# Kernel optimization log

Hardware: AMD Instinct MI355X
Metric: run time of the kernel (lower is better)

Reference implementation:

```python
import jax, jax.numpy as jnp
import numpy as np

# Module constants derived from default grid_config
D = 59          # depth bins: (60-1)/1
C_OUT = 64
X, Y, Z = 128, 128, 7
STRIDE = 16
GRID_LB = np.array([-51.2, -51.2, -2.5], dtype=np.float32)
GRID_IV = np.array([0.8, 0.8, 1.0], dtype=np.float32)
D0, DSTEP = 1.0, 1.0

B, N, C_IN, H, W = 4, 6, 256, 16, 44


def _voxel_coords():
    xs, ys, zs = np.meshgrid(np.arange(X), np.arange(Y), np.arange(Z), indexing='ij')
    coords = np.stack([xs, ys, zs], axis=-1).reshape(-1, 3).astype(np.float32)
    coords = coords * GRID_IV + GRID_LB  # [V, 3] ego-frame voxel centers
    return coords


def _camera_rig(rng):
    """Realistic 6-camera rig: yawed cameras looking outward, z_cam = forward."""
    c2e = np.zeros((B, N, 4, 4), dtype=np.float32)
    K = np.zeros((B, N, 3, 3), dtype=np.float32)
    for b in range(B):
        for n in range(N):
            a = 2.0 * np.pi * n / N + 0.02 * rng.standard_normal()
            f = np.array([np.cos(a), np.sin(a), 0.0])           # camera forward (z_cam)
            x_cam = np.array([-np.sin(a), np.cos(a), 0.0])      # camera right
            y_cam = np.array([0.0, 0.0, -1.0])                   # camera down
            R = np.stack([x_cam, y_cam, f], axis=1)              # columns = cam axes in ego
            t = 1.0 * f + np.array([0.0, 0.0, 1.5])
            c2e[b, n, :3, :3] = R
            c2e[b, n, :3, 3] = t
            c2e[b, n, 3, 3] = 1.0
            fl = 400.0 + 5.0 * rng.standard_normal()
            K[b, n] = np.array([[fl, 0.0, 352.0], [0.0, fl, 128.0], [0.0, 0.0, 1.0]])
    return c2e, K


def setup_inputs() -> dict:
    key = jax.random.key(0)
    k1, k2, k3 = jax.random.split(key, 3)
    img_feats = jax.random.normal(k1, (B, N, C_IN, H, W), dtype=jnp.float32)
    c2e, K = _camera_rig(np.random.default_rng(0))
    # depth_net: 1x1 conv in_channels -> D + C_OUT
    w_depth = jax.random.normal(k2, (D + C_OUT, C_IN), dtype=jnp.float32) * (1.0 / np.sqrt(C_IN))
    b_depth = jax.random.normal(k3, (D + C_OUT,), dtype=jnp.float32) * 0.01
    return {
        'img_feats': img_feats,
        'cam2ego': jnp.asarray(c2e),
        'cam_intrinsics': jnp.asarray(K),
        'w_depth': w_depth,
        'b_depth': b_depth,
    }


def reference(img_feats, cam2ego, cam_intrinsics, w_depth, b_depth):
    Bc, Nc, C, Hc, Wc = img_feats.shape
    # 1x1 conv == per-pixel linear
    x = jnp.einsum('bnchw,oc->bnhwo', img_feats, w_depth) + b_depth  # [B,N,H,W,D+C_OUT]
    depth = jax.nn.softmax(x[..., :D], axis=-1)                      # [B,N,H,W,D]
    feat = x[..., D:]                                                # [B,N,H,W,C_OUT]

    vox = jnp.asarray(_voxel_coords())                               # [V,3]
    V = vox.shape[0]
    vox_h = jnp.concatenate([vox, jnp.ones((V, 1), vox.dtype)], axis=1)  # [V,4]

    e2c = jnp.linalg.inv(cam2ego)                                    # [B,N,4,4]
    cam = jnp.einsum('bnij,vj->bnvi', e2c, vox_h)[..., :3]           # [B,N,V,3]
    z = cam[..., 2]
    z_safe = jnp.maximum(z, 0.1)
    norm = cam[..., :2] / z_safe[..., None]
    homo = jnp.concatenate([norm, jnp.ones_like(z[..., None])], axis=-1)  # [B,N,V,3]
    img = jnp.einsum('bnij,bnvj->bnvi', cam_intrinsics, homo)[..., :2]
    fc = img / STRIDE                                                # feature-plane coords

    depth_bin = ((z - D0) / DSTEP).astype(jnp.int32)                 # trunc toward 0, matches .long()
    valid = (
        (fc[..., 0] >= 0) & (fc[..., 0] < Wc)
        & (fc[..., 1] >= 0) & (fc[..., 1] < Hc)
        & (z > 0.5)
        & (depth_bin >= 0) & (depth_bin < D)
    )

    u = jnp.clip(fc[..., 0].astype(jnp.int32), 0, Wc - 1)            # [B,N,V]
    v = jnp.clip(fc[..., 1].astype(jnp.int32), 0, Hc - 1)
    d = jnp.clip(depth_bin, 0, D - 1)
    hw = v * Wc + u

    feat_flat = feat.reshape(Bc, Nc, Hc * Wc, C_OUT)
    sampled_feat = jnp.take_along_axis(feat_flat, hw[..., None], axis=2)   # [B,N,V,C_OUT]
    depth_flat = depth.reshape(Bc, Nc, Hc * Wc * D)
    sampled_depth = jnp.take_along_axis(depth_flat, hw * D + d, axis=2)    # [B,N,V]

    wgt = sampled_depth * valid.astype(sampled_depth.dtype)
    # scatter_add at flat_idx == voxel index (identity) -> masked sum over cameras
    bev = jnp.einsum('bnv,bnvc->bvc', wgt, sampled_feat)             # [B,V,C_OUT]
    bev = bev.reshape(Bc, X, Y, Z, C_OUT).sum(axis=3)                # collapse Z
    bev = bev.transpose(0, 3, 2, 1)                                  # [B,C_OUT,Y,X]
    return bev, depth
```

## Files before the change

### kernel.cpp

```cpp
#include <hip/hip_runtime.h>
#include <math.h>

#define D_BINS 59
#define CO     64
#define CI     256
#define NB     4
#define NC     6
#define H_IMG  16
#define W_IMG  44
#define HW     704
#define NPIX   (NB*NC*HW)
#define XD     128
#define YD     128
#define ZD     7
#define NOUT   123

__device__ void inv_rigid(const float* __restrict__ M, float* __restrict__ o) {
    double a = M[0], b = M[1], c = M[2], t0 = M[3];
    double d = M[4], e = M[5], f = M[6], t1 = M[7];
    double g = M[8], h = M[9], ii = M[10], t2 = M[11];
    double A00 = e*ii - f*h, A01 = c*h - b*ii, A02 = b*f - c*e;
    double A10 = f*g - d*ii, A11 = a*ii - c*g, A12 = c*d - a*f;
    double A20 = d*h - e*g,  A21 = b*g - a*h,  A22 = a*e - b*d;
    double det = a*A00 + b*A10 + c*A20;
    double inv = 1.0 / det;
    double r00 = A00*inv, r01 = A01*inv, r02 = A02*inv;
    double r10 = A10*inv, r11 = A11*inv, r12 = A12*inv;
    double r20 = A20*inv, r21 = A21*inv, r22 = A22*inv;
    o[0] = (float)r00; o[1] = (float)r01; o[2]  = (float)r02;
    o[3] = (float)(-(r00*t0 + r01*t1 + r02*t2));
    o[4] = (float)r10; o[5] = (float)r11; o[6]  = (float)r12;
    o[7] = (float)(-(r10*t0 + r11*t1 + r12*t2));
    o[8] = (float)r20; o[9] = (float)r21; o[10] = (float)r22;
    o[11] = (float)(-(r20*t0 + r21*t1 + r22*t2));
}

__global__ __launch_bounds__(256) void k_pre(
    const float* __restrict__ wd, const float* __restrict__ c2e,
    float* __restrict__ wt, float* __restrict__ e2c) {
    const int o = blockIdx.x;
    const int k = threadIdx.x;
    float v = (o < NOUT) ? wd[(size_t)o * CI + k] : 0.f;
    wt[(size_t)k * 128 + o] = v;
    if (blockIdx.x == 0 && k < NB * NC)
        inv_rigid(c2e + k * 16, e2c + k * 12);
}

__global__ __launch_bounds__(512) void k_head(
    const float* __restrict__ img, const float* __restrict__ wt,
    const float* __restrict__ bd, float* __restrict__ depth_out,
    float* __restrict__ feat_ws) {
    __shared__ float smem[8448 + 64];
    float* A_lds = smem;
    float* S = smem + 8448;

    const int px = threadIdx.x;
    const int tid = threadIdx.y * 64 + threadIdx.x;
    const int o0 = __builtin_amdgcn_readfirstlane(threadIdx.y << 4);
    const int p0 = blockIdx.x * 64;
    const int bn = p0 / HW;
    const int hw0 = p0 % HW;
    const float* imgb = img + (size_t)bn * CI * HW + hw0;

    float acc[16];
#pragma unroll
    for (int j = 0; j < 16; ++j) acc[j] = 0.f;

    for (int kc = 0; kc < 4; ++kc) {
#pragma unroll
        for (int it = 0; it < 2; ++it) {
            int idx = tid + it * 512;
            int r = idx >> 4, c4 = idx & 15;
            float4 v = *(const float4*)(imgb + (size_t)(kc * 64 + r) * HW + c4 * 4);
            *(float4*)(A_lds + r * 64 + c4 * 4) = v;
        }
        __syncthreads();
        const float* wr = wt + (size_t)(kc * 64) * 128 + o0;
#pragma unroll 4
        for (int k = 0; k < 64; ++k) {
            float a = A_lds[k * 64 + px];
            const float* w = wr + k * 128;
#pragma unroll
            for (int j = 0; j < 16; ++j)
                acc[j] = fmaf(a, w[j], acc[j]);
        }
        __syncthreads();
    }

    float* X = smem;
#pragma unroll
    for (int j = 0; j < 16; ++j) {
        int o = o0 + j;
        if (o < NOUT) {
            int col = (o < D_BINS) ? o : o + 5;
            X[px * 132 + col] = acc[j] + bd[o];
        }
    }
    __syncthreads();

#pragma unroll
    for (int it = 0; it < 2; ++it) {
        int g = tid + it * 512;
        int p = g >> 4, m = g & 15;
        float4 v = *(const float4*)(X + p * 132 + 64 + m * 4);
        *(float4*)(feat_ws + (size_t)(p0 + p) * CO + m * 4) = v;
    }

    if (tid < 64) {
        float* row = X + tid * 132;
        float m = row[0];
        for (int o = 1; o < D_BINS; ++o) m = fmaxf(m, row[o]);
        float s = 0.f;
        for (int o = 0; o < D_BINS; ++o) {
            float e = __expf(row[o] - m);
            row[o] = e;
            s += e;
        }
        S[tid] = 1.f / s;
    }
    __syncthreads();

    for (int g = tid; g < 64 * D_BINS; g += 512) {
        int p = g / D_BINS;
        int o = g - p * D_BINS;
        depth_out[(size_t)p0 * D_BINS + g] = X[p * 132 + o] * S[p];
    }
}

__global__ __launch_bounds__(256) void k_splat(
    const float* __restrict__ e2c, const float* __restrict__ Kmat,
    const float* __restrict__ depth_g, const float* __restrict__ feat_ws,
    float* __restrict__ bev) {
    const int tx = threadIdx.x;
    const int cq = threadIdx.y;
    const int x = blockIdx.x * 64 + tx;
    const int y = blockIdx.y;
    const int b = blockIdx.z;
    const float wx = (float)x * 0.8f + (-51.2f);
    const float wy = (float)y * 0.8f + (-51.2f);

    float acc[16];
#pragma unroll
    for (int m = 0; m < 16; ++m) acc[m] = 0.f;

    for (int n = 0; n < NC; ++n) {
        const int bn = b * NC + n;
        const float* E = e2c + bn * 12;
        const float* Km = Kmat + bn * 9;
        const float k00 = Km[0], k01 = Km[1], k02 = Km[2];
        const float k10 = Km[3], k11 = Km[4], k12 = Km[5];
        const float e02 = E[2], e12 = E[6], e22 = E[10];
        const float bx0 = E[0] * wx + E[1] * wy + E[3];
        const float bx1 = E[4] * wx + E[5] * wy + E[7];
        const float bx2 = E[8] * wx + E[9] * wy + E[11];
#pragma unroll
        for (int z = 0; z < ZD; ++z) {
            const float wz = -2.5f + (float)z;
            const float cx = bx0 + e02 * wz;
            const float cy = bx1 + e12 * wz;
            const float cz = bx2 + e22 * wz;
            const float zs = fmaxf(cz, 0.1f);
            const float rz = 1.0f / zs;
            const float xn = cx * rz;
            const float yn = cy * rz;
            const float fu = (k00 * xn + k01 * yn + k02) * 0.0625f;
            const float fv = (k10 * xn + k11 * yn + k12) * 0.0625f;
            const int bin = (int)(cz - 1.0f);
            const bool valid = (fu >= 0.f) & (fu < (float)W_IMG) &
                               (fv >= 0.f) & (fv < (float)H_IMG) &
                               (cz > 0.5f) & (bin >= 0) & (bin < D_BINS);
            if (valid) {
                int u = (int)fu;
                int v = (int)fv;
                int hw = v * W_IMG + u;
                float wgt = depth_g[((size_t)bn * HW + hw) * D_BINS + bin];
                const float4* fp =
                    (const float4*)(feat_ws + ((size_t)bn * HW + hw) * CO + cq * 16);
                float4 f0 = fp[0], f1 = fp[1], f2 = fp[2], f3 = fp[3];
                acc[0]  = fmaf(wgt, f0.x, acc[0]);
                acc[1]  = fmaf(wgt, f0.y, acc[1]);
                acc[2]  = fmaf(wgt, f0.z, acc[2]);
                acc[3]  = fmaf(wgt, f0.w, acc[3]);
                acc[4]  = fmaf(wgt, f1.x, acc[4]);
                acc[5]  = fmaf(wgt, f1.y, acc[5]);
                acc[6]  = fmaf(wgt, f1.z, acc[6]);
                acc[7]  = fmaf(wgt, f1.w, acc[7]);
                acc[8]  = fmaf(wgt, f2.x, acc[8]);
                acc[9]  = fmaf(wgt, f2.y, acc[9]);
                acc[10] = fmaf(wgt, f2.z, acc[10]);
                acc[11] = fmaf(wgt, f2.w, acc[11]);
                acc[12] = fmaf(wgt, f3.x, acc[12]);
                acc[13] = fmaf(wgt, f3.y, acc[13]);
                acc[14] = fmaf(wgt, f3.z, acc[14]);
                acc[15] = fmaf(wgt, f3.w, acc[15]);
            }
        }
    }
    float* ob = bev + (((size_t)b * CO + cq * 16) * YD + y) * XD + x;
#pragma unroll
    for (int m = 0; m < 16; ++m) ob[(size_t)m * YD * XD] = acc[m];
}

extern "C" void kernel_launch(void* const* d_in, const int* in_sizes, int n_in,
                              void* d_out, int out_size, void* d_ws, size_t ws_size,
                              hipStream_t stream) {
    const float* img  = (const float*)d_in[0];
    const float* c2e  = (const float*)d_in[1];
    const float* Kmat = (const float*)d_in[2];
    const float* wd   = (const float*)d_in[3];
    const float* bd   = (const float*)d_in[4];
    float* bev = (float*)d_out;
    float* depth_out = bev + (size_t)NB * CO * YD * XD;
    float* feat_ws = (float*)d_ws;
    float* wt  = feat_ws + (size_t)NPIX * CO;
    float* e2c = wt + 256 * 128;

    k_pre<<<128, 256, 0, stream>>>(wd, c2e, wt, e2c);
    k_head<<<NPIX / 64, dim3(64, 8, 1), 0, stream>>>(img, wt, bd, depth_out, feat_ws);
    k_splat<<<dim3(2, YD, NB), dim3(64, 4, 1), 0, stream>>>(e2c, Kmat, depth_out,
                                                            feat_ws, bev);
}
```

Baseline: 130.7 us.

## Retile head to 66 pixels per block and give splat threads 32 channels

```diff
diff --git a/kernel.cpp b/kernel.cpp
--- a/kernel.cpp
+++ b/kernel.cpp
@@ -14,6 +14,7 @@
 #define YD     128
 #define ZD     7
 #define NOUT   123
+#define PXB    66
 
 __device__ void inv_rigid(const float* __restrict__ M, float* __restrict__ o) {
     double a = M[0], b = M[1], c = M[2], t0 = M[3];
@@ -46,67 +47,91 @@
         inv_rigid(c2e + k * 16, e2c + k * 12);
 }
 
-__global__ __launch_bounds__(512) void k_head(
+__global__ __launch_bounds__(640) void k_head(
     const float* __restrict__ img, const float* __restrict__ wt,
     const float* __restrict__ bd, float* __restrict__ depth_out,
     float* __restrict__ feat_ws) {
-    __shared__ float smem[8448 + 64];
-    float* A_lds = smem;
-    float* S = smem + 8448;
-
-    const int px = threadIdx.x;
-    const int tid = threadIdx.y * 64 + threadIdx.x;
-    const int o0 = __builtin_amdgcn_readfirstlane(threadIdx.y << 4);
-    const int p0 = blockIdx.x * 64;
-    const int bn = p0 / HW;
-    const int hw0 = p0 % HW;
-    const float* imgb = img + (size_t)bn * CI * HW + hw0;
+    __shared__ float smem[PXB * 132 + PXB];
+    float* S = smem + PXB * 132;
+
+    const int tid = threadIdx.x;
+    const int wv  = tid >> 6;
+    const int ln  = tid & 63;
+    const int p0  = blockIdx.x * PXB;
+    const bool is_main = (wv < 8);
+    const int o0  = __builtin_amdgcn_readfirstlane((is_main ? wv : 0) << 4);
+    const int epx = 64 + (wv - 8);
 
     float acc[16];
 #pragma unroll
     for (int j = 0; j < 16; ++j) acc[j] = 0.f;
+    float acc2[2] = {0.f, 0.f};
 
     for (int kc = 0; kc < 4; ++kc) {
 #pragma unroll
-        for (int it = 0; it < 2; ++it) {
-            int idx = tid + it * 512;
-            int r = idx >> 4, c4 = idx & 15;
-            float4 v = *(const float4*)(imgb + (size_t)(kc * 64 + r) * HW + c4 * 4);
-            *(float4*)(A_lds + r * 64 + c4 * 4) = v;
+        for (int it = 0; it < 7; ++it) {
+            int idx = tid + it * 640;
+            if (idx < 64 * PXB) {
+                int kl = idx / PXB, px = idx - kl * PXB;
+                int p = p0 + px;
+                int bn = p / HW, hw = p - bn * HW;
+                smem[kl * PXB + px] =
+                    img[((size_t)bn * CI + kc * 64 + kl) * HW + hw];
+            }
         }
         __syncthreads();
-        const float* wr = wt + (size_t)(kc * 64) * 128 + o0;
+        if (is_main) {
+            const float* wr = wt + (size_t)(kc * 64) * 128 + o0;
 #pragma unroll 4
-        for (int k = 0; k < 64; ++k) {
-            float a = A_lds[k * 64 + px];
-            const float* w = wr + k * 128;
-#pragma unroll
-            for (int j = 0; j < 16; ++j)
-                acc[j] = fmaf(a, w[j], acc[j]);
+            for (int k = 0; k < 64; ++k) {
+                float a = smem[k * PXB + ln];
+                const float* w = wr + k * 128;
+#pragma unroll
+                for (int j = 0; j < 16; ++j)
+                    acc[j] = fmaf(a, w[j], acc[j]);
+            }
+        } else {
+#pragma unroll 4
+            for (int k = 0; k < 64; ++k) {
+                float a = smem[k * PXB + epx];
+                const float* w = wt + (size_t)(kc * 64 + k) * 128;
+                acc2[0] = fmaf(a, w[ln], acc2[0]);
+                acc2[1] = fmaf(a, w[ln + 64], acc2[1]);
+            }
         }
         __syncthreads();
     }
 
     float* X = smem;
-#pragma unroll
-    for (int j = 0; j < 16; ++j) {
-        int o = o0 + j;
-        if (o < NOUT) {
-            int col = (o < D_BINS) ? o : o + 5;
-            X[px * 132 + col] = acc[j] + bd[o];
-        }
+    if (is_main) {
+#pragma unroll
+        for (int j = 0; j < 16; ++j) {
+            int o = o0 + j;
+            if (o < NOUT) {
+                int col = (o < D_BINS) ? o : o + 5;
+                X[ln * 132 + col] = acc[j] + bd[o];
+            }
+        }
+    } else {
+        int o = ln;
+        X[epx * 132 + ((o < D_BINS) ? o : o + 5)] = acc2[0] + bd[o];
+        o = ln + 64;
+        if (o < NOUT)
+            X[epx * 132 + ((o < D_BINS) ? o : o + 5)] = acc2[1] + bd[o];
     }
     __syncthreads();
 
 #pragma unroll
     for (int it = 0; it < 2; ++it) {
-        int g = tid + it * 512;
-        int p = g >> 4, m = g & 15;
-        float4 v = *(const float4*)(X + p * 132 + 64 + m * 4);
-        *(float4*)(feat_ws + (size_t)(p0 + p) * CO + m * 4) = v;
-    }
-
-    if (tid < 64) {
+        int g = tid + it * 640;
+        if (g < PXB * 16) {
+            int p = g >> 4, m = g & 15;
+            float4 v = *(const float4*)(X + p * 132 + 64 + m * 4);
+            *(float4*)(feat_ws + (size_t)(p0 + p) * CO + m * 4) = v;
+        }
+    }
+
+    if (tid < PXB) {
         float* row = X + tid * 132;
         float m = row[0];
         for (int o = 1; o < D_BINS; ++o) m = fmaxf(m, row[o]);
@@ -120,7 +145,7 @@
     }
     __syncthreads();
 
-    for (int g = tid; g < 64 * D_BINS; g += 512) {
+    for (int g = tid; g < PXB * D_BINS; g += 640) {
         int p = g / D_BINS;
         int o = g - p * D_BINS;
         depth_out[(size_t)p0 * D_BINS + g] = X[p * 132 + o] * S[p];
@@ -131,17 +156,18 @@
     const float* __restrict__ e2c, const float* __restrict__ Kmat,
     const float* __restrict__ depth_g, const float* __restrict__ feat_ws,
     float* __restrict__ bev) {
-    const int tx = threadIdx.x;
-    const int cq = threadIdx.y;
+    const int tx   = threadIdx.x;
+    const int half = threadIdx.y & 1;
+    const int yq   = threadIdx.y >> 1;
     const int x = blockIdx.x * 64 + tx;
-    const int y = blockIdx.y;
+    const int y = blockIdx.y * 2 + yq;
     const int b = blockIdx.z;
     const float wx = (float)x * 0.8f + (-51.2f);
     const float wy = (float)y * 0.8f + (-51.2f);
 
-    float acc[16];
-#pragma unroll
-    for (int m = 0; m < 16; ++m) acc[m] = 0.f;
+    float acc[32];
+#pragma unroll
+    for (int m = 0; m < 32; ++m) acc[m] = 0.f;
 
     for (int n = 0; n < NC; ++n) {
         const int bn = b * NC + n;
@@ -175,30 +201,21 @@
                 int hw = v * W_IMG + u;
                 float wgt = depth_g[((size_t)bn * HW + hw) * D_BINS + bin];
                 const float4* fp =
-                    (const float4*)(feat_ws + ((size_t)bn * HW + hw) * CO + cq * 16);
-                float4 f0 = fp[0], f1 = fp[1], f2 = fp[2], f3 = fp[3];
-                acc[0]  = fmaf(wgt, f0.x, acc[0]);
-                acc[1]  = fmaf(wgt, f0.y, acc[1]);
-                acc[2]  = fmaf(wgt, f0.z, acc[2]);
-                acc[3]  = fmaf(wgt, f0.w, acc[3]);
-                acc[4]  = fmaf(wgt, f1.x, acc[4]);
-                acc[5]  = fmaf(wgt, f1.y, acc[5]);
-                acc[6]  = fmaf(wgt, f1.z, acc[6]);
-                acc[7]  = fmaf(wgt, f1.w, acc[7]);
-                acc[8]  = fmaf(wgt, f2.x, acc[8]);
-                acc[9]  = fmaf(wgt, f2.y, acc[9]);
-                acc[10] = fmaf(wgt, f2.z, acc[10]);
-                acc[11] = fmaf(wgt, f2.w, acc[11]);
-                acc[12] = fmaf(wgt, f3.x, acc[12]);
-                acc[13] = fmaf(wgt, f3.y, acc[13]);
-                acc[14] = fmaf(wgt, f3.z, acc[14]);
-                acc[15] = fmaf(wgt, f3.w, acc[15]);
-            }
-        }
-    }
-    float* ob = bev + (((size_t)b * CO + cq * 16) * YD + y) * XD + x;
-#pragma unroll
-    for (int m = 0; m < 16; ++m) ob[(size_t)m * YD * XD] = acc[m];
+                    (const float4*)(feat_ws + ((size_t)bn * HW + hw) * CO + half * 32);
+#pragma unroll
+                for (int q = 0; q < 8; ++q) {
+                    float4 f = fp[q];
+                    acc[q * 4 + 0] = fmaf(wgt, f.x, acc[q * 4 + 0]);
+                    acc[q * 4 + 1] = fmaf(wgt, f.y, acc[q * 4 + 1]);
+                    acc[q * 4 + 2] = fmaf(wgt, f.z, acc[q * 4 + 2]);
+                    acc[q * 4 + 3] = fmaf(wgt, f.w, acc[q * 4 + 3]);
+                }
+            }
+        }
+    }
+    float* ob = bev + (((size_t)b * CO + half * 32) * YD + y) * XD + x;
+#pragma unroll
+    for (int m = 0; m < 32; ++m) ob[(size_t)m * YD * XD] = acc[m];
 }
 
 extern "C" void kernel_launch(void* const* d_in, const int* in_sizes, int n_in,
@@ -216,7 +233,7 @@
     float* e2c = wt + 256 * 128;
 
     k_pre<<<128, 256, 0, stream>>>(wd, c2e, wt, e2c);
-    k_head<<<NPIX / 64, dim3(64, 8, 1), 0, stream>>>(img, wt, bd, depth_out, feat_ws);
-    k_splat<<<dim3(2, YD, NB), dim3(64, 4, 1), 0, stream>>>(e2c, Kmat, depth_out,
+    k_head<<<256, 640, 0, stream>>>(img, wt, bd, depth_out, feat_ws);
+    k_splat<<<dim3(2, 64, NB), dim3(64, 4, 1), 0, stream>>>(e2c, Kmat, depth_out,
                                                             feat_ws, bev);
 }
```

New measurement: 132.1 us. Within noise of the previous version (+1.1%).
